# Kernel tuning notes

Hardware: AMD Instinct MI355X
Metric: run time of the kernel (lower is better)

The kernel has to match this reference:

```python
import jax, jax.numpy as jnp
import numpy as np
import math


def _dct_kernel():
    # Fixed 4x4 2D-DCT basis, 16 output filters, shape (16, 1, 4, 4) in OIHW.
    u = np.full(4, math.sqrt(2.0 / 4.0), dtype=np.float32)
    u[0] = math.sqrt(1.0 / 4.0)
    k = np.zeros((16, 1, 4, 4), dtype=np.float32)
    for kk in range(4):
        for ll in range(4):
            for i in range(4):
                for j in range(4):
                    k[kk * 4 + ll, 0, i, j] = (
                        u[kk] * u[ll]
                        * math.cos(math.pi / 8.0 * kk * (2 * i + 1))
                        * math.cos(math.pi / 8.0 * ll * (2 * j + 1))
                    )
    return jnp.asarray(k)


def setup_inputs() -> dict:
    key = jax.random.key(0)
    x = jax.random.normal(key, (8, 3, 512, 512), dtype=jnp.float32)
    return {"x": x}


def reference(x):
    B, C, H, W = x.shape
    dct = _dct_kernel()                       # (16, 1, 4, 4)
    kernel = jnp.tile(dct, (C, 1, 1, 1))      # (16*C, 1, 4, 4), grouped conv
    # Per-channel conv with the same fixed DCT kernel == grouped conv with
    # feature_group_count=C. padding=2 on a 4x4 kernel -> H+1, W+1 output.
    out = jax.lax.conv_general_dilated(
        x, kernel,
        window_strides=(1, 1),
        padding=[(2, 2), (2, 2)],
        dimension_numbers=("NCHW", "OIHW", "NCHW"),
        feature_group_count=C,
    )  # (B, 16*C, H+1, W+1)
    # DCT_Trunc(|out|) = -(relu(-|out|+8)-8) = min(|out|, 8)
    return jnp.minimum(jnp.abs(out), 8.0)
```

## Files before the change

kernel.cpp:

```cpp
#include <hip/hip_runtime.h>


#define IHW 512
#define OHW 513

__global__ __launch_bounds__(256) void dct_layer_kernel(
    const float* __restrict__ x, float* __restrict__ out) {
    const float A1 = 0.6532814824381883f;
    const float A2 = 0.2705980500730985f;

    int pix = blockIdx.x * 256 + threadIdx.x;
    if (pix >= OHW * OHW) return;
    int oh = pix / OHW;
    int ow = pix - oh * OHW;
    int bc = blockIdx.y;

    const float* __restrict__ xin = x + (size_t)bc * (IHW * IHW);

    float p[4][4];
#pragma unroll
    for (int i = 0; i < 4; ++i) {
        int ih = oh - 2 + i;
        bool rv = ((unsigned)ih < (unsigned)IHW);
        const float* row = xin + ih * IHW;
#pragma unroll
        for (int j = 0; j < 4; ++j) {
            int iw = ow - 2 + j;
            bool ok = rv && ((unsigned)iw < (unsigned)IHW);
            p[i][j] = ok ? row[iw] : 0.0f;
        }
    }

    float t[4][4];
#pragma unroll
    for (int j = 0; j < 4; ++j) {
        float s03 = p[0][j] + p[3][j];
        float d03 = p[0][j] - p[3][j];
        float s12 = p[1][j] + p[2][j];
        float d12 = p[1][j] - p[2][j];
        t[0][j] = 0.5f * (s03 + s12);
        t[1][j] = A1 * d03 + A2 * d12;
        t[2][j] = 0.5f * (s03 - s12);
        t[3][j] = A2 * d03 - A1 * d12;
    }

    float r[16];
#pragma unroll
    for (int kk = 0; kk < 4; ++kk) {
        float s03 = t[kk][0] + t[kk][3];
        float d03 = t[kk][0] - t[kk][3];
        float s12 = t[kk][1] + t[kk][2];
        float d12 = t[kk][1] - t[kk][2];
        r[kk * 4 + 0] = 0.5f * (s03 + s12);
        r[kk * 4 + 1] = A1 * d03 + A2 * d12;
        r[kk * 4 + 2] = 0.5f * (s03 - s12);
        r[kk * 4 + 3] = A2 * d03 - A1 * d12;
    }

    const size_t PLANE = (size_t)OHW * OHW;
    size_t obase = (size_t)bc * 16 * PLANE + (size_t)pix;
#pragma unroll
    for (int c = 0; c < 16; ++c) {
        out[obase + (size_t)c * PLANE] = fminf(fabsf(r[c]), 8.0f);
    }
}

extern "C" void kernel_launch(void* const* d_in, const int* in_sizes, int n_in,
                              void* d_out, int out_size, void* d_ws, size_t ws_size,
                              hipStream_t stream) {
    const float* x = (const float*)d_in[0];
    float* out = (float*)d_out;
    dim3 grid((OHW * OHW + 255) / 256, 24);
    hipLaunchKernelGGL(dct_layer_kernel, grid, dim3(256), 0, stream, x, out);
}
```

Baseline: 458.8 us.

## Share vertical DCT pass via LDS across row-tiled blocks, split edge column

Each block now handles one output row segment of 256 columns. Every thread computes the vertical 4-point DCT for one input column and stores it in shared memory, so the horizontal pass reuses neighbours' partial results instead of each thread loading and transforming a full 4x4 patch. The last output column (ow=512) is handled by a separate small kernel, which adds a second launch. The kernel is dominated by output writes of about 400MB, so the saving in loads and ALU work may be small next to store bandwidth. Output indexing now uses 32-bit unsigned arithmetic, which still fits the output size.

```diff
diff --git a/kernel.cpp b/kernel.cpp
--- a/kernel.cpp
+++ b/kernel.cpp
@@ -1,67 +1,104 @@
 #include <hip/hip_runtime.h>
 
 
-#define IHW 512
-#define OHW 513
+#define IW 512
+#define PLANE 263169u
 
-__global__ __launch_bounds__(256) void dct_layer_kernel(
-    const float* __restrict__ x, float* __restrict__ out) {
+__device__ __forceinline__ float4 vtrans(const float* __restrict__ xin,
+                                         int c, int ih0) {
     const float A1 = 0.6532814824381883f;
     const float A2 = 0.2705980500730985f;
+    float p0 = 0.f, p1 = 0.f, p2 = 0.f, p3 = 0.f;
+    if ((unsigned)c < (unsigned)IW) {
+        const float* col = xin + c;
+        if ((unsigned)(ih0 + 0) < (unsigned)IW) p0 = col[(ih0 + 0) * IW];
+        if ((unsigned)(ih0 + 1) < (unsigned)IW) p1 = col[(ih0 + 1) * IW];
+        if ((unsigned)(ih0 + 2) < (unsigned)IW) p2 = col[(ih0 + 2) * IW];
+        if ((unsigned)(ih0 + 3) < (unsigned)IW) p3 = col[(ih0 + 3) * IW];
+    }
+    float s03 = p0 + p3, d03 = p0 - p3, s12 = p1 + p2, d12 = p1 - p2;
+    return make_float4(0.5f * (s03 + s12), A1 * d03 + A2 * d12,
+                       0.5f * (s03 - s12), A2 * d03 - A1 * d12);
+}
 
-    int pix = blockIdx.x * 256 + threadIdx.x;
-    if (pix >= OHW * OHW) return;
-    int oh = pix / OHW;
-    int ow = pix - oh * OHW;
-    int bc = blockIdx.y;
+__global__ __launch_bounds__(256) void dct_main(const float* __restrict__ x,
+                                                float* __restrict__ out) {
+    const float A1 = 0.6532814824381883f;
+    const float A2 = 0.2705980500730985f;
+    __shared__ float4 tc[259];
 
-    const float* __restrict__ xin = x + (size_t)bc * (IHW * IHW);
+    int tid  = threadIdx.x;
+    int base = blockIdx.x << 8;
+    int oh   = blockIdx.y;
+    int bc   = blockIdx.z;
+    const float* xin = x + (size_t)bc * (IW * IW);
+    int ih0 = oh - 2;
 
-    float p[4][4];
+    float4 own = vtrans(xin, base + tid, ih0);
+    tc[tid + 2] = own;
+    if (tid < 3) {
+        int idx = (tid < 2) ? tid : 258;
+        int c   = (tid < 2) ? (base - 2 + tid) : (base + 256);
+        tc[idx] = vtrans(xin, c, ih0);
+    }
+    __syncthreads();
+
+    float4 t0 = tc[tid];
+    float4 t1 = tc[tid + 1];
+    float4 t3 = tc[tid + 3];
+
+    unsigned obase = (unsigned)bc * (16u * PLANE) + (unsigned)oh * 513u
+                   + (unsigned)(base + tid);
+
+    float c0[4] = {t0.x, t0.y, t0.z, t0.w};
+    float c1[4] = {t1.x, t1.y, t1.z, t1.w};
+    float c2[4] = {own.x, own.y, own.z, own.w};
+    float c3[4] = {t3.x, t3.y, t3.z, t3.w};
+
 #pragma unroll
-    for (int i = 0; i < 4; ++i) {
-        int ih = oh - 2 + i;
-        bool rv = ((unsigned)ih < (unsigned)IHW);
-        const float* row = xin + ih * IHW;
+    for (int m = 0; m < 4; ++m) {
+        float s03 = c0[m] + c3[m], d03 = c0[m] - c3[m];
+        float s12 = c1[m] + c2[m], d12 = c1[m] - c2[m];
+        float r0 = 0.5f * (s03 + s12);
+        float r1 = A1 * d03 + A2 * d12;
+        float r2 = 0.5f * (s03 - s12);
+        float r3 = A2 * d03 - A1 * d12;
+        out[obase + (unsigned)(m * 4 + 0) * PLANE] = fminf(fabsf(r0), 8.0f);
+        out[obase + (unsigned)(m * 4 + 1) * PLANE] = fminf(fabsf(r1), 8.0f);
+        out[obase + (unsigned)(m * 4 + 2) * PLANE] = fminf(fabsf(r2), 8.0f);
+        out[obase + (unsigned)(m * 4 + 3) * PLANE] = fminf(fabsf(r3), 8.0f);
+    }
+}
+
+__global__ __launch_bounds__(256) void dct_edge(const float* __restrict__ x,
+                                                float* __restrict__ out) {
+    const float A1 = 0.6532814824381883f;
+    const float A2 = 0.2705980500730985f;
+    int g = blockIdx.x * 256 + threadIdx.x;
+    if (g >= 24 * 513) return;
+    int bc = g / 513;
+    int oh = g - bc * 513;
+    const float* xin = x + (size_t)bc * (IW * IW);
+    int ih0 = oh - 2;
+
+    float4 t0 = vtrans(xin, 510, ih0);
+    float4 t1 = vtrans(xin, 511, ih0);
+    float c0[4] = {t0.x, t0.y, t0.z, t0.w};
+    float c1[4] = {t1.x, t1.y, t1.z, t1.w};
+
+    unsigned obase = (unsigned)bc * (16u * PLANE) + (unsigned)oh * 513u + 512u;
 #pragma unroll
-        for (int j = 0; j < 4; ++j) {
-            int iw = ow - 2 + j;
-            bool ok = rv && ((unsigned)iw < (unsigned)IHW);
-            p[i][j] = ok ? row[iw] : 0.0f;
-        }
-    }
-
-    float t[4][4];
-#pragma unroll
-    for (int j = 0; j < 4; ++j) {
-        float s03 = p[0][j] + p[3][j];
-        float d03 = p[0][j] - p[3][j];
-        float s12 = p[1][j] + p[2][j];
-        float d12 = p[1][j] - p[2][j];
-        t[0][j] = 0.5f * (s03 + s12);
-        t[1][j] = A1 * d03 + A2 * d12;
-        t[2][j] = 0.5f * (s03 - s12);
-        t[3][j] = A2 * d03 - A1 * d12;
-    }
-
-    float r[16];
-#pragma unroll
-    for (int kk = 0; kk < 4; ++kk) {
-        float s03 = t[kk][0] + t[kk][3];
-        float d03 = t[kk][0] - t[kk][3];
-        float s12 = t[kk][1] + t[kk][2];
-        float d12 = t[kk][1] - t[kk][2];
-        r[kk * 4 + 0] = 0.5f * (s03 + s12);
-        r[kk * 4 + 1] = A1 * d03 + A2 * d12;
-        r[kk * 4 + 2] = 0.5f * (s03 - s12);
-        r[kk * 4 + 3] = A2 * d03 - A1 * d12;
-    }
-
-    const size_t PLANE = (size_t)OHW * OHW;
-    size_t obase = (size_t)bc * 16 * PLANE + (size_t)pix;
-#pragma unroll
-    for (int c = 0; c < 16; ++c) {
-        out[obase + (size_t)c * PLANE] = fminf(fabsf(r[c]), 8.0f);
+    for (int m = 0; m < 4; ++m) {
+        float s03 = c0[m], d03 = c0[m];
+        float s12 = c1[m], d12 = c1[m];
+        float r0 = 0.5f * (s03 + s12);
+        float r1 = A1 * d03 + A2 * d12;
+        float r2 = 0.5f * (s03 - s12);
+        float r3 = A2 * d03 - A1 * d12;
+        out[obase + (unsigned)(m * 4 + 0) * PLANE] = fminf(fabsf(r0), 8.0f);
+        out[obase + (unsigned)(m * 4 + 1) * PLANE] = fminf(fabsf(r1), 8.0f);
+        out[obase + (unsigned)(m * 4 + 2) * PLANE] = fminf(fabsf(r2), 8.0f);
+        out[obase + (unsigned)(m * 4 + 3) * PLANE] = fminf(fabsf(r3), 8.0f);
     }
 }
 
@@ -70,6 +107,9 @@
                               hipStream_t stream) {
     const float* x = (const float*)d_in[0];
     float* out = (float*)d_out;
-    dim3 grid((OHW * OHW + 255) / 256, 24);
-    hipLaunchKernelGGL(dct_layer_kernel, grid, dim3(256), 0, stream, x, out);
+    dim3 grid(2, 513, 24);
+    hipLaunchKernelGGL(dct_main, grid, dim3(256), 0, stream, x, out);
+    int edge_threads = 24 * 513;
+    hipLaunchKernelGGL(dct_edge, dim3((edge_threads + 255) / 256), dim3(256), 0,
+                       stream, x, out);
 }
```

After: 474.8 us. 1.03x slower.
